# Kernel optimization log

Measured on AMD Instinct MI355X. Metric: run time of the kernel, lower is better.

## Reference

```python
import jax, jax.numpy as jnp
import numpy as np


def setup_inputs() -> dict:
    key = jax.random.key(0)
    ks = jax.random.split(key, 5)
    B, S, H, E, F = 2, 2048, 2048, 8, 2048
    return {
        "hidden_states": jax.random.normal(ks[0], (B, S, H), dtype=jnp.float32),
        "gate_w": jax.random.normal(ks[1], (E, H), dtype=jnp.float32) * 0.02,
        "w1s": jax.random.normal(ks[2], (E, H, F), dtype=jnp.float32) * 0.02,
        "w2s": jax.random.normal(ks[3], (E, F, H), dtype=jnp.float32) * 0.02,
        "w3s": jax.random.normal(ks[4], (E, H, F), dtype=jnp.float32) * 0.02,
        "top_k": 2,
    }


def reference(hidden_states, gate_w, w1s, w2s, w3s, top_k):
    B, S, H = hidden_states.shape
    E = gate_w.shape[0]
    x = hidden_states.reshape(-1, H)               # [T, H]
    T = x.shape[0]
    # Router: softmax in fp32, top-k, renormalize (matches torch F.softmax(dtype=float))
    logits = x @ gate_w.T                          # [T, E]
    probs = jax.nn.softmax(logits.astype(jnp.float32), axis=-1)
    topw, topi = jax.lax.top_k(probs, top_k)       # [T, k]
    topw = topw / jnp.sum(topw, axis=-1, keepdims=True)
    # Dense combine weights [T, E]: zero for unselected experts.
    combine = jnp.zeros((T, E), dtype=x.dtype)
    combine = combine.at[jnp.arange(T)[:, None], topi].add(topw.astype(x.dtype))
    # Expert FFN (SwiGLU): silu(x @ w1) * (x @ w3) @ w2, per expert.
    h1 = jnp.einsum("th,ehf->etf", x, w1s)         # [E, T, F]
    h3 = jnp.einsum("th,ehf->etf", x, w3s)
    h = jax.nn.silu(h1) * h3
    out_e = jnp.einsum("etf,efh->eth", h, w2s)      # [E, T, H]
    out = jnp.einsum("eth,te->th", out_e, combine)  # weighted merge
    return out.reshape(B, S, H)
```

## Files before the change

### kernel.cpp

```cpp
#include <hip/hip_runtime.h>
#include <cstdint>
#include <cstddef>

#define Tt 4096
#define Hd 2048
#define Fd 2048
#define En 8
#define Rcap 9216

typedef short bf16x8 __attribute__((ext_vector_type(8)));
typedef float f32x4 __attribute__((ext_vector_type(4)));
typedef unsigned int u32;
typedef u32 __attribute__((address_space(1))) gas_u32;
typedef u32 __attribute__((address_space(3))) las_u32;

__device__ __forceinline__ unsigned short f2bf(float f) {
    u32 u = __builtin_bit_cast(u32, f);
    u = (u + 0x7FFFu + ((u >> 16) & 1u)) >> 16;
    return (unsigned short)u;
}
__device__ __forceinline__ float bf2f(unsigned short s) {
    return __builtin_bit_cast(float, ((u32)s) << 16);
}

__global__ __launch_bounds__(256) void router_kernel(
    const float* __restrict__ x, const float* __restrict__ gate,
    int* __restrict__ topi, float* __restrict__ topw)
{
    const int t = blockIdx.x;
    const float* xr = x + (size_t)t * Hd;
    float acc[En];
    #pragma unroll
    for (int e = 0; e < En; ++e) acc[e] = 0.f;
    for (int h = threadIdx.x; h < Hd; h += 256) {
        const float xv = xr[h];
        #pragma unroll
        for (int e = 0; e < En; ++e) acc[e] += xv * gate[e * Hd + h];
    }
    #pragma unroll
    for (int e = 0; e < En; ++e) {
        float v = acc[e];
        for (int d = 32; d > 0; d >>= 1) v += __shfl_down(v, d, 64);
        acc[e] = v;
    }
    __shared__ float red[En][4];
    const int lane = threadIdx.x & 63, wv = threadIdx.x >> 6;
    if (lane == 0) {
        #pragma unroll
        for (int e = 0; e < En; ++e) red[e][wv] = acc[e];
    }
    __syncthreads();
    if (threadIdx.x == 0) {
        float l[En];
        #pragma unroll
        for (int e = 0; e < En; ++e) l[e] = red[e][0] + red[e][1] + red[e][2] + red[e][3];
        float m = l[0];
        #pragma unroll
        for (int e = 1; e < En; ++e) m = fmaxf(m, l[e]);
        float p[En];
        #pragma unroll
        for (int e = 0; e < En; ++e) p[e] = expf(l[e] - m);
        int i1 = 0;
        #pragma unroll
        for (int e = 1; e < En; ++e) if (p[e] > p[i1]) i1 = e;
        int i2 = (i1 == 0) ? 1 : 0;
        #pragma unroll
        for (int e = 0; e < En; ++e) if (e != i1 && p[e] > p[i2]) i2 = e;
        const float s = p[i1] + p[i2];
        topi[2 * t] = i1; topi[2 * t + 1] = i2;
        topw[2 * t] = p[i1] / s; topw[2 * t + 1] = p[i2] / s;
    }
}

__global__ void assign_kernel(const int* __restrict__ topi, int* __restrict__ cnt,
                              int* __restrict__ posbuf)
{
    const int idx = blockIdx.x * blockDim.x + threadIdx.x;
    if (idx >= Tt * 2) return;
    posbuf[idx] = atomicAdd(&cnt[topi[idx]], 1);
}

__global__ void scan_kernel(const int* __restrict__ cnt, int* __restrict__ off,
                            int* __restrict__ pcnt)
{
    if (threadIdx.x == 0 && blockIdx.x == 0) {
        int a = 0;
        for (int e = 0; e < En; ++e) {
            off[e] = a;
            const int pc = (cnt[e] + 127) & ~127;
            pcnt[e] = pc;
            a += pc;
        }
    }
}

__global__ __launch_bounds__(256) void gather_kernel(
    const float* __restrict__ x, const int* __restrict__ topi,
    const float* __restrict__ topw, const int* __restrict__ off,
    const int* __restrict__ posbuf, unsigned short* __restrict__ Xg,
    int* __restrict__ tokrow, float* __restrict__ wrow)
{
    const int entry = blockIdx.x;
    const int t = entry >> 1;
    const int e = topi[entry];
    const int row = off[e] + posbuf[entry];
    if (threadIdx.x == 0) { tokrow[row] = t; wrow[row] = topw[entry]; }
    const float4* src = (const float4*)(x + (size_t)t * Hd);
    const int i = threadIdx.x;
    const float4 a = src[2 * i], b = src[2 * i + 1];
    unsigned short o[8];
    o[0] = f2bf(a.x); o[1] = f2bf(a.y); o[2] = f2bf(a.z); o[3] = f2bf(a.w);
    o[4] = f2bf(b.x); o[5] = f2bf(b.y); o[6] = f2bf(b.z); o[7] = f2bf(b.w);
    ((uint4*)(Xg + (size_t)row * Hd))[i] = *(const uint4*)o;
}

__global__ __launch_bounds__(256) void transpose_kernel(
    const float* __restrict__ w1s, const float* __restrict__ w3s,
    const float* __restrict__ w2s, unsigned short* __restrict__ w1T,
    unsigned short* __restrict__ w3T, unsigned short* __restrict__ w2T)
{
    __shared__ float tile[32][33];
    const int z = blockIdx.z, tensor = z >> 3, e = z & 7;
    const float* src = (tensor == 0) ? w1s : (tensor == 1) ? w3s : w2s;
    unsigned short* dst = (tensor == 0) ? w1T : (tensor == 1) ? w3T : w2T;
    const int c0 = blockIdx.x * 32, r0 = blockIdx.y * 32;
    const int tx = threadIdx.x & 31, ty = threadIdx.x >> 5;
    const size_t base = (size_t)e * 2048 * 2048;
    #pragma unroll
    for (int r = 0; r < 4; ++r)
        tile[ty + r * 8][tx] = src[base + (size_t)(r0 + ty + r * 8) * 2048 + c0 + tx];
    __syncthreads();
    #pragma unroll
    for (int r = 0; r < 4; ++r)
        dst[base + (size_t)(c0 + ty + r * 8) * 2048 + r0 + tx] = f2bf(tile[tx][ty + r * 8]);
}

template <int EPI>
__global__ __launch_bounds__(256) void gemm_kernel(
    const unsigned short* __restrict__ Ab,
    const unsigned short* __restrict__ Bb0,
    const unsigned short* __restrict__ Bb1,
    unsigned short* __restrict__ C0,
    unsigned short* __restrict__ C1,
    float* __restrict__ outp,
    const int* __restrict__ off, const int* __restrict__ pcnt,
    const int* __restrict__ tokrow, const float* __restrict__ wrow)
{
    const int z = blockIdx.z;
    const int e = (EPI == 0) ? (z >> 1) : z;
    const int mt = blockIdx.y;
    const int pc = pcnt[e];
    if (mt * 128 >= pc) return;
    const int nt = blockIdx.x;
    const int row0 = off[e] + mt * 128;

    const unsigned short* A = Ab + (size_t)row0 * 2048;
    const unsigned short* Bsel = (EPI == 0 && (z & 1)) ? Bb1 : Bb0;
    const unsigned short* B = Bsel + (size_t)e * 2048 * 2048 + (size_t)nt * 128 * 2048;

    __shared__ __align__(16) unsigned short As[128 * 64];
    __shared__ __align__(16) unsigned short Bs[128 * 64];

    const int tid = threadIdx.x;
    const int lane = tid & 63;
    const int wv = tid >> 6;
    const int wm = wv & 1, wn = wv >> 1;
    const int quad = lane >> 4, l16 = lane & 15;

    f32x4 acc[4][4];
    const f32x4 zero4 = {0.f, 0.f, 0.f, 0.f};
    #pragma unroll
    for (int i = 0; i < 4; ++i)
        #pragma unroll
        for (int j = 0; j < 4; ++j) acc[i][j] = zero4;

    for (int kt = 0; kt < 2048; kt += 64) {
        __syncthreads();
        #pragma unroll
        for (int i = 0; i < 4; ++i) {
            const int grp = i * 4 + wv;
            const int idx = grp * 64 + lane;
            const int r = idx >> 3;
            const int kc = (idx & 7) ^ (r & 7);
            const unsigned short* ga = A + (size_t)r * 2048 + kt + kc * 8;
            __builtin_amdgcn_global_load_lds((const gas_u32*)ga,
                                             (las_u32*)(As + grp * 512), 16, 0, 0);
            const unsigned short* gb = B + (size_t)r * 2048 + kt + kc * 8;
            __builtin_amdgcn_global_load_lds((const gas_u32*)gb,
                                             (las_u32*)(Bs + grp * 512), 16, 0, 0);
        }
        __syncthreads();
        #pragma unroll
        for (int ks = 0; ks < 2; ++ks) {
            bf16x8 af[4], bfr[4];
            #pragma unroll
            for (int mi = 0; mi < 4; ++mi) {
                const int m = wm * 64 + mi * 16 + l16;
                const int ck = ks * 4 + quad;
                const int slot = m * 8 + (ck ^ (m & 7));
                af[mi] = *(const bf16x8*)(As + slot * 8);
            }
            #pragma unroll
            for (int ni = 0; ni < 4; ++ni) {
                const int n = wn * 64 + ni * 16 + l16;
                const int ck = ks * 4 + quad;
                const int slot = n * 8 + (ck ^ (n & 7));
                bfr[ni] = *(const bf16x8*)(Bs + slot * 8);
            }
            #pragma unroll
            for (int mi = 0; mi < 4; ++mi)
                #pragma unroll
                for (int ni = 0; ni < 4; ++ni)
                    acc[mi][ni] = __builtin_amdgcn_mfma_f32_16x16x32_bf16(
                        af[mi], bfr[ni], acc[mi][ni], 0, 0, 0);
        }
    }

    if (EPI == 0) {
        unsigned short* C = (z & 1) ? C1 : C0;
        #pragma unroll
        for (int mi = 0; mi < 4; ++mi) {
            const int rbase = row0 + wm * 64 + mi * 16 + quad * 4;
            #pragma unroll
            for (int ni = 0; ni < 4; ++ni) {
                const int col = nt * 128 + wn * 64 + ni * 16 + l16;
                #pragma unroll
                for (int r = 0; r < 4; ++r)
                    C[(size_t)(rbase + r) * 2048 + col] = f2bf(acc[mi][ni][r]);
            }
        }
    } else {
        #pragma unroll
        for (int mi = 0; mi < 4; ++mi) {
            const int rbase = row0 + wm * 64 + mi * 16 + quad * 4;
            #pragma unroll
            for (int r = 0; r < 4; ++r) {
                const int rg = rbase + r;
                const int t = tokrow[rg];
                const float w = wrow[rg];
                float* orow = outp + (size_t)t * 2048 + nt * 128 + wn * 64;
                #pragma unroll
                for (int ni = 0; ni < 4; ++ni)
                    unsafeAtomicAdd(orow + ni * 16 + l16, acc[mi][ni][r] * w);
            }
        }
    }
}

__global__ __launch_bounds__(256) void silumul_kernel(
    unsigned short* __restrict__ H1buf, const unsigned short* __restrict__ H3buf)
{
    const size_t idx = ((size_t)blockIdx.x * 256 + threadIdx.x) * 8;
    uint4 h1 = *(const uint4*)(H1buf + idx);
    const uint4 h3 = *(const uint4*)(H3buf + idx);
    unsigned short* p1 = (unsigned short*)&h1;
    const unsigned short* p3 = (const unsigned short*)&h3;
    #pragma unroll
    for (int j = 0; j < 8; ++j) {
        const float a = bf2f(p1[j]);
        const float b = bf2f(p3[j]);
        const float s = a / (1.f + expf(-a));
        p1[j] = f2bf(s * b);
    }
    *(uint4*)(H1buf + idx) = h1;
}

static constexpr size_t SZ_WT  = (size_t)En * 2048 * 2048 * 2;
static constexpr size_t SZ_XG  = (size_t)Rcap * 2048 * 2;
static constexpr size_t O_W1T  = 0;
static constexpr size_t O_W3T  = O_W1T + SZ_WT;
static constexpr size_t O_W2T  = O_W3T + SZ_WT;
static constexpr size_t O_XG   = O_W2T + SZ_WT;
static constexpr size_t O_H1   = O_XG + SZ_XG;
static constexpr size_t O_H3   = O_H1 + SZ_XG;
static constexpr size_t O_TOPI = O_H3 + SZ_XG;
static constexpr size_t O_TOPW = O_TOPI + (size_t)Tt * 2 * 4;
static constexpr size_t O_POS  = O_TOPW + (size_t)Tt * 2 * 4;
static constexpr size_t O_OFF  = O_POS + (size_t)Tt * 2 * 4;
static constexpr size_t O_PCNT = O_OFF + 64;
static constexpr size_t O_CNT  = O_PCNT + 64;
static constexpr size_t O_TOKROW = O_CNT + 64;
static constexpr size_t O_WROW = O_TOKROW + (size_t)Rcap * 4;
static constexpr size_t ZERO_SZ = 64 + (size_t)Rcap * 4 + (size_t)Rcap * 4;

extern "C" void kernel_launch(void* const* d_in, const int* in_sizes, int n_in,
                              void* d_out, int out_size, void* d_ws, size_t ws_size,
                              hipStream_t stream)
{
    const float* x    = (const float*)d_in[0];
    const float* gate = (const float*)d_in[1];
    const float* w1s  = (const float*)d_in[2];
    const float* w2s  = (const float*)d_in[3];
    const float* w3s  = (const float*)d_in[4];
    float* out = (float*)d_out;
    char* ws = (char*)d_ws;

    unsigned short* w1T = (unsigned short*)(ws + O_W1T);
    unsigned short* w3T = (unsigned short*)(ws + O_W3T);
    unsigned short* w2T = (unsigned short*)(ws + O_W2T);
    unsigned short* Xg  = (unsigned short*)(ws + O_XG);
    unsigned short* H1  = (unsigned short*)(ws + O_H1);
    unsigned short* H3  = (unsigned short*)(ws + O_H3);
    int*   topi   = (int*)(ws + O_TOPI);
    float* topw   = (float*)(ws + O_TOPW);
    int*   posbuf = (int*)(ws + O_POS);
    int*   off    = (int*)(ws + O_OFF);
    int*   pcnt   = (int*)(ws + O_PCNT);
    int*   cnt    = (int*)(ws + O_CNT);
    int*   tokrow = (int*)(ws + O_TOKROW);
    float* wrow   = (float*)(ws + O_WROW);

    hipMemsetAsync(out, 0, (size_t)Tt * Hd * 4, stream);
    hipMemsetAsync(ws + O_XG, 0, SZ_XG, stream);
    hipMemsetAsync(ws + O_CNT, 0, ZERO_SZ, stream);

    transpose_kernel<<<dim3(64, 64, 24), 256, 0, stream>>>(w1s, w3s, w2s, w1T, w3T, w2T);
    router_kernel<<<Tt, 256, 0, stream>>>(x, gate, topi, topw);
    assign_kernel<<<(Tt * 2) / 256, 256, 0, stream>>>(topi, cnt, posbuf);
    scan_kernel<<<1, 64, 0, stream>>>(cnt, off, pcnt);
    gather_kernel<<<Tt * 2, 256, 0, stream>>>(x, topi, topw, off, posbuf, Xg, tokrow, wrow);

    gemm_kernel<0><<<dim3(16, 32, 16), 256, 0, stream>>>(
        Xg, w1T, w3T, H1, H3, nullptr, off, pcnt, tokrow, wrow);
    silumul_kernel<<<(Rcap * Fd) / 2048, 256, 0, stream>>>(H1, H3);
    gemm_kernel<1><<<dim3(16, 32, 8), 256, 0, stream>>>(
        H1, w2T, nullptr, nullptr, nullptr, out, off, pcnt, tokrow, wrow);
}
```

Before: 881.0 us.

## Replace atomic scatter with fp32 staging buffer and merge kernel; widen transpose tiles

The down-projection GEMM now writes plain fp32 rows into a staging buffer that reuses the w1T workspace, which is dead by then. A new merge kernel then combines each token's two expert rows with their routing weights. This removes the atomic adds, the output memset and the tokrow/wrow bookkeeping, at the cost of an extra fp32 write and read of about 75MB. The GEMM grid is flattened to row tiles that look up their expert from the offsets, so blocks past the padded rows exit early. The weight transpose moves to 64x64 tiles with float4 loads and 16-byte stores.

```diff
diff --git a/kernel.cpp b/kernel.cpp
--- a/kernel.cpp
+++ b/kernel.cpp
@@ -96,15 +96,13 @@
 
 __global__ __launch_bounds__(256) void gather_kernel(
     const float* __restrict__ x, const int* __restrict__ topi,
-    const float* __restrict__ topw, const int* __restrict__ off,
-    const int* __restrict__ posbuf, unsigned short* __restrict__ Xg,
-    int* __restrict__ tokrow, float* __restrict__ wrow)
+    const int* __restrict__ off, const int* __restrict__ posbuf,
+    unsigned short* __restrict__ Xg)
 {
     const int entry = blockIdx.x;
     const int t = entry >> 1;
     const int e = topi[entry];
     const int row = off[e] + posbuf[entry];
-    if (threadIdx.x == 0) { tokrow[row] = t; wrow[row] = topw[entry]; }
     const float4* src = (const float4*)(x + (size_t)t * Hd);
     const int i = threadIdx.x;
     const float4 a = src[2 * i], b = src[2 * i + 1];
@@ -119,20 +117,33 @@
     const float* __restrict__ w2s, unsigned short* __restrict__ w1T,
     unsigned short* __restrict__ w3T, unsigned short* __restrict__ w2T)
 {
-    __shared__ float tile[32][33];
+    __shared__ float tile[64][65];
     const int z = blockIdx.z, tensor = z >> 3, e = z & 7;
     const float* src = (tensor == 0) ? w1s : (tensor == 1) ? w3s : w2s;
     unsigned short* dst = (tensor == 0) ? w1T : (tensor == 1) ? w3T : w2T;
-    const int c0 = blockIdx.x * 32, r0 = blockIdx.y * 32;
-    const int tx = threadIdx.x & 31, ty = threadIdx.x >> 5;
+    const int c0 = blockIdx.x * 64, r0 = blockIdx.y * 64;
     const size_t base = (size_t)e * 2048 * 2048;
-    #pragma unroll
-    for (int r = 0; r < 4; ++r)
-        tile[ty + r * 8][tx] = src[base + (size_t)(r0 + ty + r * 8) * 2048 + c0 + tx];
+
+    {
+        const int r = threadIdx.x >> 2, cg = (threadIdx.x & 3) * 16;
+        const float4* s4 = (const float4*)(src + base + (size_t)(r0 + r) * 2048 + c0 + cg);
+        #pragma unroll
+        for (int i = 0; i < 4; ++i) {
+            const float4 v = s4[i];
+            float* tr = &tile[r][cg + 4 * i];
+            tr[0] = v.x; tr[1] = v.y; tr[2] = v.z; tr[3] = v.w;
+        }
+    }
     __syncthreads();
-    #pragma unroll
-    for (int r = 0; r < 4; ++r)
-        dst[base + (size_t)(c0 + ty + r * 8) * 2048 + r0 + tx] = f2bf(tile[tx][ty + r * 8]);
+    {
+        const int ny = threadIdx.x >> 2, k0 = (threadIdx.x & 3) * 16;
+        __align__(16) unsigned short o[16];
+        #pragma unroll
+        for (int j = 0; j < 16; ++j) o[j] = f2bf(tile[k0 + j][ny]);
+        unsigned short* d = dst + base + (size_t)(c0 + ny) * 2048 + r0 + k0;
+        *(uint4*)(d) = *(const uint4*)(o);
+        *(uint4*)(d + 8) = *(const uint4*)(o + 8);
+    }
 }
 
 template <int EPI>
@@ -142,20 +153,18 @@
     const unsigned short* __restrict__ Bb1,
     unsigned short* __restrict__ C0,
     unsigned short* __restrict__ C1,
-    float* __restrict__ outp,
-    const int* __restrict__ off, const int* __restrict__ pcnt,
-    const int* __restrict__ tokrow, const float* __restrict__ wrow)
-{
-    const int z = blockIdx.z;
-    const int e = (EPI == 0) ? (z >> 1) : z;
-    const int mt = blockIdx.y;
-    const int pc = pcnt[e];
-    if (mt * 128 >= pc) return;
+    float* __restrict__ Cf,
+    const int* __restrict__ off, const int* __restrict__ pcnt)
+{
+    const int row0 = blockIdx.y * 128;
+    int e = 0;
+    #pragma unroll
+    for (int i = 1; i < En; ++i) if (row0 >= off[i]) e = i;
+    if (row0 >= off[e] + pcnt[e]) return;
     const int nt = blockIdx.x;
-    const int row0 = off[e] + mt * 128;
 
     const unsigned short* A = Ab + (size_t)row0 * 2048;
-    const unsigned short* Bsel = (EPI == 0 && (z & 1)) ? Bb1 : Bb0;
+    const unsigned short* Bsel = (EPI == 0 && blockIdx.z) ? Bb1 : Bb0;
     const unsigned short* B = Bsel + (size_t)e * 2048 * 2048 + (size_t)nt * 128 * 2048;
 
     __shared__ __align__(16) unsigned short As[128 * 64];
@@ -217,7 +226,7 @@
     }
 
     if (EPI == 0) {
-        unsigned short* C = (z & 1) ? C1 : C0;
+        unsigned short* C = blockIdx.z ? C1 : C0;
         #pragma unroll
         for (int mi = 0; mi < 4; ++mi) {
             const int rbase = row0 + wm * 64 + mi * 16 + quad * 4;
@@ -234,14 +243,11 @@
         for (int mi = 0; mi < 4; ++mi) {
             const int rbase = row0 + wm * 64 + mi * 16 + quad * 4;
             #pragma unroll
-            for (int r = 0; r < 4; ++r) {
-                const int rg = rbase + r;
-                const int t = tokrow[rg];
-                const float w = wrow[rg];
-                float* orow = outp + (size_t)t * 2048 + nt * 128 + wn * 64;
+            for (int ni = 0; ni < 4; ++ni) {
+                const int col = nt * 128 + wn * 64 + ni * 16 + l16;
                 #pragma unroll
-                for (int ni = 0; ni < 4; ++ni)
-                    unsafeAtomicAdd(orow + ni * 16 + l16, acc[mi][ni][r] * w);
+                for (int r = 0; r < 4; ++r)
+                    Cf[(size_t)(rbase + r) * 2048 + col] = acc[mi][ni][r];
             }
         }
     }
@@ -263,6 +269,31 @@
         p1[j] = f2bf(s * b);
     }
     *(uint4*)(H1buf + idx) = h1;
+}
+
+__global__ __launch_bounds__(256) void merge_kernel(
+    const float* __restrict__ Yg, const int* __restrict__ topi,
+    const float* __restrict__ topw, const int* __restrict__ off,
+    const int* __restrict__ posbuf, float* __restrict__ out)
+{
+    const int t = blockIdx.x;
+    const int rowA = off[topi[2 * t]] + posbuf[2 * t];
+    const int rowB = off[topi[2 * t + 1]] + posbuf[2 * t + 1];
+    const float wA = topw[2 * t], wB = topw[2 * t + 1];
+    const int c = threadIdx.x * 8;
+    const float4* pa = (const float4*)(Yg + (size_t)rowA * 2048 + c);
+    const float4* pb = (const float4*)(Yg + (size_t)rowB * 2048 + c);
+    float4* po = (float4*)(out + (size_t)t * 2048 + c);
+    #pragma unroll
+    for (int i = 0; i < 2; ++i) {
+        const float4 a = pa[i], b = pb[i];
+        float4 o;
+        o.x = wA * a.x + wB * b.x;
+        o.y = wA * a.y + wB * b.y;
+        o.z = wA * a.z + wB * b.z;
+        o.w = wA * a.w + wB * b.w;
+        po[i] = o;
+    }
 }
 
 static constexpr size_t SZ_WT  = (size_t)En * 2048 * 2048 * 2;
@@ -279,9 +310,6 @@
 static constexpr size_t O_OFF  = O_POS + (size_t)Tt * 2 * 4;
 static constexpr size_t O_PCNT = O_OFF + 64;
 static constexpr size_t O_CNT  = O_PCNT + 64;
-static constexpr size_t O_TOKROW = O_CNT + 64;
-static constexpr size_t O_WROW = O_TOKROW + (size_t)Rcap * 4;
-static constexpr size_t ZERO_SZ = 64 + (size_t)Rcap * 4 + (size_t)Rcap * 4;
 
 extern "C" void kernel_launch(void* const* d_in, const int* in_sizes, int n_in,
                               void* d_out, int out_size, void* d_ws, size_t ws_size,
@@ -301,28 +329,27 @@
     unsigned short* Xg  = (unsigned short*)(ws + O_XG);
     unsigned short* H1  = (unsigned short*)(ws + O_H1);
     unsigned short* H3  = (unsigned short*)(ws + O_H3);
+    float* Yg     = (float*)(ws + O_W1T);
     int*   topi   = (int*)(ws + O_TOPI);
     float* topw   = (float*)(ws + O_TOPW);
     int*   posbuf = (int*)(ws + O_POS);
     int*   off    = (int*)(ws + O_OFF);
     int*   pcnt   = (int*)(ws + O_PCNT);
     int*   cnt    = (int*)(ws + O_CNT);
-    int*   tokrow = (int*)(ws + O_TOKROW);
-    float* wrow   = (float*)(ws + O_WROW);
-
-    hipMemsetAsync(out, 0, (size_t)Tt * Hd * 4, stream);
+
     hipMemsetAsync(ws + O_XG, 0, SZ_XG, stream);
-    hipMemsetAsync(ws + O_CNT, 0, ZERO_SZ, stream);
-
-    transpose_kernel<<<dim3(64, 64, 24), 256, 0, stream>>>(w1s, w3s, w2s, w1T, w3T, w2T);
+    hipMemsetAsync(ws + O_CNT, 0, 64, stream);
+
+    transpose_kernel<<<dim3(32, 32, 24), 256, 0, stream>>>(w1s, w3s, w2s, w1T, w3T, w2T);
     router_kernel<<<Tt, 256, 0, stream>>>(x, gate, topi, topw);
     assign_kernel<<<(Tt * 2) / 256, 256, 0, stream>>>(topi, cnt, posbuf);
     scan_kernel<<<1, 64, 0, stream>>>(cnt, off, pcnt);
-    gather_kernel<<<Tt * 2, 256, 0, stream>>>(x, topi, topw, off, posbuf, Xg, tokrow, wrow);
-
-    gemm_kernel<0><<<dim3(16, 32, 16), 256, 0, stream>>>(
-        Xg, w1T, w3T, H1, H3, nullptr, off, pcnt, tokrow, wrow);
+    gather_kernel<<<Tt * 2, 256, 0, stream>>>(x, topi, off, posbuf, Xg);
+
+    gemm_kernel<0><<<dim3(16, 72, 2), 256, 0, stream>>>(
+        Xg, w1T, w3T, H1, H3, nullptr, off, pcnt);
     silumul_kernel<<<(Rcap * Fd) / 2048, 256, 0, stream>>>(H1, H3);
-    gemm_kernel<1><<<dim3(16, 32, 8), 256, 0, stream>>>(
-        H1, w2T, nullptr, nullptr, nullptr, out, off, pcnt, tokrow, wrow);
-}
+    gemm_kernel<1><<<dim3(16, 72, 1), 256, 0, stream>>>(
+        H1, w2T, nullptr, nullptr, nullptr, Yg, off, pcnt);
+    merge_kernel<<<Tt, 256, 0, stream>>>(Yg, topi, topw, off, posbuf, out);
+}
```

Result: faster. 821.3 us (-6.8%).
